# Kernel optimization log

Hardware: AMD Instinct MI355X
Metric: run time of the kernel (lower is better)

The kernel has to match this reference:

```python
import jax, jax.numpy as jnp
import numpy as np

D_MODEL = 1024
N_HEADS = 16
D_KV = 64
B, S = 2, 2048


def setup_inputs() -> dict:
    key = jax.random.key(0)
    ks = jax.random.split(key, 7)
    scale = 1.0 / np.sqrt(D_MODEL)
    return {
        "query": jax.random.normal(ks[0], (B, S, D_MODEL), jnp.float32),
        "key": jax.random.normal(ks[1], (B, S, D_MODEL), jnp.float32),
        "value": jax.random.normal(ks[2], (B, S, D_MODEL), jnp.float32),
        "mask": jnp.zeros((B, 1, 1, S), jnp.float32),
        "Wq": jax.random.normal(ks[3], (D_MODEL, N_HEADS * D_KV), jnp.float32) * scale,
        "Wk": jax.random.normal(ks[4], (D_MODEL, N_HEADS * D_KV), jnp.float32) * scale,
        "Wv": jax.random.normal(ks[5], (D_MODEL, N_HEADS * D_KV), jnp.float32) * scale,
        "Wo": jax.random.normal(ks[6], (N_HEADS * D_KV, D_MODEL), jnp.float32) * scale,
    }


def _split_heads(x):
    b, s, _ = x.shape
    return x.reshape(b, s, N_HEADS, D_KV).transpose(0, 2, 1, 3)  # [B,H,S,Dk]


def reference(query, key, value, mask, Wq, Wk, Wv, Wo):
    q = _split_heads(query @ Wq)
    k = _split_heads(key @ Wk)
    v = _split_heads(value @ Wv)
    scores = jnp.einsum("bhqd,bhkd->bhqk", q, k) / jnp.sqrt(
        jnp.asarray(D_KV, scores_dtype := q.dtype)
    )
    scores = scores + mask
    attn = jax.nn.softmax(scores, axis=-1)  # dropout_rate=0 -> identity
    ctx = jnp.einsum("bhqk,bhkd->bhqd", attn, v)
    ctx = ctx.transpose(0, 2, 1, 3).reshape(query.shape[0], -1, N_HEADS * D_KV)
    hidden = ctx @ Wo
    return hidden
```

## Files before the change

kernel.cpp:

```cpp
#include <hip/hip_runtime.h>
#include <hip/hip_bf16.h>
#include <stdint.h>

typedef __bf16 bf16;
typedef __bf16 bf16x8 __attribute__((ext_vector_type(8)));
typedef __bf16 bf16x4 __attribute__((ext_vector_type(4)));
typedef float  f32x4  __attribute__((ext_vector_type(4)));
typedef float  f32x16 __attribute__((ext_vector_type(16)));

#define S_LEN  2048
#define NH     16
#define DKV    64
#define DMODEL 1024
#define LOG2E  1.4426950408889634f

__device__ __forceinline__ void async_load16(const void* g, void* l) {
  __builtin_amdgcn_global_load_lds(
      (const __attribute__((address_space(1))) uint32_t*)(uintptr_t)g,
      (__attribute__((address_space(3))) uint32_t*)(uintptr_t)l,
      16, 0, 0);
}

__global__ void cast_qkv(const float* __restrict__ q, const float* __restrict__ k,
                         const float* __restrict__ v,
                         bf16* __restrict__ qo, bf16* __restrict__ ko, bf16* __restrict__ vo)
{
  int z = blockIdx.y;
  const float* in = (z == 0) ? q : (z == 1) ? k : v;
  bf16* out = (z == 0) ? qo : (z == 1) ? ko : vo;
  int i = blockIdx.x * 256 + threadIdx.x;
  const float4* in4 = (const float4*)in;
  float4 a = in4[2 * i];
  float4 c = in4[2 * i + 1];
  bf16x8 o;
  o[0] = (bf16)a.x; o[1] = (bf16)a.y; o[2] = (bf16)a.z; o[3] = (bf16)a.w;
  o[4] = (bf16)c.x; o[5] = (bf16)c.y; o[6] = (bf16)c.z; o[7] = (bf16)c.w;
  ((bf16x8*)out)[i] = o;
}

__global__ void transpose_w(const float* __restrict__ W0, const float* __restrict__ W1,
                            const float* __restrict__ W2, const float* __restrict__ W3,
                            bf16* __restrict__ T0, bf16* __restrict__ T1,
                            bf16* __restrict__ T2, bf16* __restrict__ T3)
{
  int z = blockIdx.z;
  const float* W = (z == 0) ? W0 : (z == 1) ? W1 : (z == 2) ? W2 : W3;
  bf16* T = (z == 0) ? T0 : (z == 1) ? T1 : (z == 2) ? T2 : T3;
  __shared__ float tile[32][33];
  int n0 = blockIdx.x * 32, k0 = blockIdx.y * 32;
  int tx = threadIdx.x, ty = threadIdx.y;
  for (int i = 0; i < 32; i += 8)
    tile[ty + i][tx] = W[(size_t)(k0 + ty + i) * DMODEL + n0 + tx];
  __syncthreads();
  for (int i = 0; i < 32; i += 8)
    T[(size_t)(n0 + ty + i) * DMODEL + k0 + tx] = (bf16)tile[tx][ty + i];
}

template<int TM, int MODE>
__global__ __launch_bounds__(256) void gemm_bt(
    const bf16* __restrict__ A0, const bf16* __restrict__ A1, const bf16* __restrict__ A2,
    const bf16* __restrict__ B0, const bf16* __restrict__ B1, const bf16* __restrict__ B2,
    void* __restrict__ C0, void* __restrict__ C1, void* __restrict__ C2,
    int M, int N, int K)
{
  constexpr int MI = TM / 32;
  __shared__ __align__(16) bf16 As[TM * 32];
  __shared__ __align__(16) bf16 Bs[128 * 32];
  int z = blockIdx.z;
  const bf16* A  = (z == 0) ? A0 : (z == 1) ? A1 : A2;
  const bf16* Bt = (z == 0) ? B0 : (z == 1) ? B1 : B2;
  void* C        = (z == 0) ? C0 : (z == 1) ? C1 : C2;

  const int m0 = blockIdx.y * TM;
  const int n0 = blockIdx.x * 128;
  const int tid = threadIdx.x;
  const int lane = tid & 63;
  const int wave = tid >> 6;
  const int wm = (wave >> 1) * (TM / 2);
  const int wn = (wave & 1) * 64;
  const int row = lane & 15;
  const int quad = lane >> 4;

  f32x4 acc[MI][4];
  for (int i = 0; i < MI; ++i)
    for (int j = 0; j < 4; ++j) acc[i][j] = (f32x4){0.f, 0.f, 0.f, 0.f};

  const int nk = K >> 5;
  for (int kt = 0; kt < nk; ++kt) {
    __syncthreads();
    const int kk = kt << 5;
    for (int j = 0; j < TM / 64; ++j) {
      int base = j * 256 + wave * 64;
      int idx = base + lane;
      int r = idx >> 2;
      int cb = (idx & 3) << 4;
      async_load16((const char*)(A + (size_t)(m0 + r) * K + kk) + cb,
                   (char*)As + (size_t)base * 16);
    }
    for (int j = 0; j < 2; ++j) {
      int base = j * 256 + wave * 64;
      int idx = base + lane;
      int r = idx >> 2;
      int cb = (idx & 3) << 4;
      async_load16((const char*)(Bt + (size_t)(n0 + r) * K + kk) + cb,
                   (char*)Bs + (size_t)base * 16);
    }
    __syncthreads();
    bf16x8 af[MI], bfr[4];
    for (int i = 0; i < MI; ++i)
      af[i] = *(const bf16x8*)(As + (wm + i * 16 + row) * 32 + quad * 8);
    for (int j = 0; j < 4; ++j)
      bfr[j] = *(const bf16x8*)(Bs + (wn + j * 16 + row) * 32 + quad * 8);
    for (int i = 0; i < MI; ++i)
      for (int j = 0; j < 4; ++j)
        acc[i][j] = __builtin_amdgcn_mfma_f32_16x16x32_bf16(af[i], bfr[j], acc[i][j], 0, 0, 0);
  }

  if (MODE == 0) {
    float* Cf = (float*)C;
    for (int i = 0; i < MI; ++i)
      for (int j = 0; j < 4; ++j)
        for (int r = 0; r < 4; ++r) {
          int gm = m0 + wm + i * 16 + quad * 4 + r;
          int gn = n0 + wn + j * 16 + row;
          Cf[(size_t)gm * N + gn] = acc[i][j][r];
        }
  } else if (z != 2) {
    bf16* Cb = (bf16*)C;
    for (int i = 0; i < MI; ++i)
      for (int j = 0; j < 4; ++j)
        for (int r = 0; r < 4; ++r) {
          int gm = m0 + wm + i * 16 + quad * 4 + r;
          int gn = n0 + wn + j * 16 + row;
          int b = gm >> 11, s = gm & 2047;
          int h = gn >> 6,  d = gn & 63;
          Cb[(((size_t)(b * NH + h)) * S_LEN + s) * DKV + d] = (bf16)acc[i][j][r];
        }
  } else {
    bf16* Cb = (bf16*)C;
    for (int i = 0; i < MI; ++i)
      for (int j = 0; j < 4; ++j) {
        int gm = m0 + wm + i * 16 + quad * 4;
        int gn = n0 + wn + j * 16 + row;
        int b = gm >> 11, s = gm & 2047;
        int h = gn >> 6,  d = gn & 63;
        int bh = b * NH + h;
        int tile = s >> 6, kb = (s & 63) >> 2;
        bf16x4 t;
        for (int r = 0; r < 4; ++r) t[r] = (bf16)acc[i][j][r];
        *(bf16x4*)(Cb + ((((size_t)bh * 32 + tile) * 16 + kb) * 64 + d) * 4) = t;
      }
  }
}

__global__ __launch_bounds__(256, 4) void attn_kernel(
    const bf16* __restrict__ Qh, const bf16* __restrict__ Kh, const bf16* __restrict__ Vperm,
    const float* __restrict__ mask, float* __restrict__ Opart, float* __restrict__ Lpart)
{
  __shared__ __align__(16) bf16 Ks[64 * 64];
  __shared__ __align__(16) bf16 Vts[64 * 64];
  __shared__ __align__(16) float masks2[64];

  const int bh = blockIdx.y;
  const int b = bh >> 4;
  const int q0 = blockIdx.x * 128;
  const int zh = blockIdx.z;
  const int tid = threadIdx.x;
  const int lane = tid & 63;
  const int wave = tid >> 6;
  const int ln = lane & 31;
  const int hi = lane >> 5;
  const float SC2 = 0.125f * LOG2E;

  const int qg = q0 + wave * 32 + ln;
  bf16x8 qf[4];
  {
    const bf16* qrow = Qh + ((size_t)bh * S_LEN + qg) * DKV;
    for (int c = 0; c < 4; ++c)
      qf[c] = *(const bf16x8*)(qrow + c * 16 + hi * 8);
  }

  f32x16 O[2];
  for (int nb = 0; nb < 2; ++nb)
    for (int i = 0; i < 16; ++i) O[nb][i] = 0.f;
  float lsum = 0.f;

  for (int it = 0; it < 16; ++it) {
    const int kv0 = zh * 1024 + it * 64;
    __syncthreads();
    const bf16* vtile = Vperm + ((size_t)bh * 32 + (kv0 >> 6)) * (64 * 64);
    for (int j = 0; j < 2; ++j) {
      int base = j * 256 + wave * 64;
      int idx = base + lane;
      int r = idx >> 3;
      int cc = (idx & 7) ^ (r & 7);
      async_load16(Kh + ((size_t)bh * S_LEN + kv0 + r) * DKV + cc * 8,
                   (char*)Ks + (size_t)base * 16);
      async_load16(vtile + (size_t)idx * 8,
                   (char*)Vts + (size_t)base * 16);
    }
    if (tid < 64) masks2[tid] = mask[b * S_LEN + kv0 + tid] * LOG2E;
    __syncthreads();

    f32x16 Sm[2];
    for (int i = 0; i < 16; ++i) { Sm[0][i] = 0.f; Sm[1][i] = 0.f; }
    for (int c = 0; c < 4; ++c) {
      bf16x8 k0 = *(const bf16x8*)(Ks + ln * 64        + (((2 * c + hi) ^ (ln & 7)) << 3));
      bf16x8 k1 = *(const bf16x8*)(Ks + (32 + ln) * 64 + (((2 * c + hi) ^ (ln & 7)) << 3));
      Sm[0] = __builtin_amdgcn_mfma_f32_32x32x16_bf16(k0, qf[c], Sm[0], 0, 0, 0);
      Sm[1] = __builtin_amdgcn_mfma_f32_32x32x16_bf16(k1, qf[c], Sm[1], 0, 0, 0);
    }

    for (int cg = 0; cg < 4; ++cg) {
      int mb = cg >> 1, g = cg & 1;
      int koff = 32 * mb + 16 * g + 4 * hi;
      f32x4 mklo = *(const f32x4*)(masks2 + koff);
      f32x4 mkhi = *(const f32x4*)(masks2 + koff + 8);
      bf16x8 ap;
      float ls0 = 0.f;
      for (int u = 0; u < 4; ++u) {
        float p = __builtin_amdgcn_exp2f(Sm[mb][g * 8 + u] * SC2 + mklo[u]);
        ls0 += p; ap[u] = (bf16)p;
      }
      for (int u = 0; u < 4; ++u) {
        float p = __builtin_amdgcn_exp2f(Sm[mb][g * 8 + 4 + u] * SC2 + mkhi[u]);
        ls0 += p; ap[4 + u] = (bf16)p;
      }
      lsum += ls0;
      int kb0 = hi + 4 * g + 8 * mb;
      for (int nb = 0; nb < 2; ++nb) {
        int d = nb * 32 + ln;
        bf16x4 lo = *(const bf16x4*)(Vts + ((size_t)kb0 * 64 + d) * 4);
        bf16x4 hv = *(const bf16x4*)(Vts + ((size_t)(kb0 + 2) * 64 + d) * 4);
        bf16x8 bv;
        for (int u = 0; u < 4; ++u) { bv[u] = lo[u]; bv[u + 4] = hv[u]; }
        O[nb] = __builtin_amdgcn_mfma_f32_32x32x16_bf16(ap, bv, O[nb], 0, 0, 0);
      }
    }
  }

  float lt = lsum + __shfl_xor(lsum, 32, 64);
  if (lane < 32)
    Lpart[((size_t)zh * 32 + bh) * S_LEN + q0 + wave * 32 + ln] = lt;

  float* ob = Opart + (((size_t)zh * 32 + bh) * S_LEN) * DKV;
  for (int g = 0; g < 4; ++g)
    for (int nb = 0; nb < 2; ++nb)
      for (int j = 0; j < 4; ++j) {
        int qrow = q0 + wave * 32 + j + 8 * g + 4 * hi;
        ob[(size_t)qrow * DKV + nb * 32 + ln] = O[nb][g * 4 + j];
      }
}

__global__ void combine_kernel(const float* __restrict__ Opart,
                               const float* __restrict__ Lpart,
                               bf16* __restrict__ ctx)
{
  int t = blockIdx.x * 256 + threadIdx.x;
  int dg = t & 15;
  int q  = (t >> 4) & 2047;
  int bh = t >> 15;
  int b = bh >> 4, h = bh & 15;
  size_t o0 = ((size_t)bh * S_LEN + q) * DKV + dg * 4;
  size_t o1 = ((size_t)(32 + bh) * S_LEN + q) * DKV + dg * 4;
  f32x4 a = *(const f32x4*)(Opart + o0);
  f32x4 c = *(const f32x4*)(Opart + o1);
  float l = Lpart[(size_t)bh * S_LEN + q] + Lpart[(size_t)(32 + bh) * S_LEN + q];
  float r = 1.0f / l;
  bf16x4 o;
  for (int u = 0; u < 4; ++u) o[u] = (bf16)((a[u] + c[u]) * r);
  *(bf16x4*)(ctx + ((size_t)(b * S_LEN + q)) * DMODEL + h * DKV + dg * 4) = o;
}

extern "C" void kernel_launch(void* const* d_in, const int* in_sizes, int n_in,
                              void* d_out, int out_size, void* d_ws, size_t ws_size,
                              hipStream_t stream)
{
  const float* query = (const float*)d_in[0];
  const float* key_  = (const float*)d_in[1];
  const float* value = (const float*)d_in[2];
  const float* mask  = (const float*)d_in[3];
  const float* Wq = (const float*)d_in[4];
  const float* Wk = (const float*)d_in[5];
  const float* Wv = (const float*)d_in[6];
  const float* Wo = (const float*)d_in[7];

  char* ws = (char*)d_ws;
  const size_t MB = (size_t)1 << 20;
  bf16* qb    = (bf16*)(ws + 0 * MB);
  bf16* kb    = (bf16*)(ws + 8 * MB);
  bf16* vb    = (bf16*)(ws + 16 * MB);
  bf16* wqt   = (bf16*)(ws + 24 * MB);
  bf16* wkt   = (bf16*)(ws + 26 * MB);
  bf16* wvt   = (bf16*)(ws + 28 * MB);
  bf16* qh    = (bf16*)(ws + 32 * MB);
  bf16* kh    = (bf16*)(ws + 40 * MB);
  bf16* vperm = (bf16*)(ws + 48 * MB);
  bf16* wot   = (bf16*)(ws + 56 * MB);
  float* Opart = (float*)(ws + 0 * MB);
  float* Lpart = (float*)(ws + 58 * MB);
  bf16* ctx   = (bf16*)(ws + 32 * MB);

  cast_qkv<<<dim3(2048, 3), 256, 0, stream>>>(query, key_, value, qb, kb, vb);
  transpose_w<<<dim3(32, 32, 4), dim3(32, 8), 0, stream>>>(Wq, Wk, Wv, Wo, wqt, wkt, wvt, wot);
  gemm_bt<128, 1><<<dim3(8, 32, 3), 256, 0, stream>>>(qb, kb, vb, wqt, wkt, wvt,
                                                      (void*)qh, (void*)kh, (void*)vperm,
                                                      4096, 1024, 1024);
  attn_kernel<<<dim3(16, 32, 2), 256, 0, stream>>>(qh, kh, vperm, mask, Opart, Lpart);
  combine_kernel<<<dim3(4096), 256, 0, stream>>>(Opart, Lpart, ctx);
  gemm_bt<64, 0><<<dim3(8, 64, 1), 256, 0, stream>>>(ctx, ctx, ctx, wot, wot, wot,
                                                     d_out, d_out, d_out,
                                                     4096, 1024, 1024);
}
```

Measured before the change: 231.4 us.

## Fuse split-KV combine into attention block and stage Q/K GEMM stores via LDS

The attention kernel now runs both KV halves inside one 512-thread block, one group of four waves per half. It combines the partial outputs and row sums through shared memory and writes normalized bf16 context directly. This removes the fp32 Opart/Lpart round trip through global memory and the separate combine kernel launch. Separately, the Q/K projection epilogue stages tiles in LDS so it can issue 16-byte coalesced stores into the head-split layout instead of scattered 2-byte writes. In exchange the attention grid has half as many blocks, each using more LDS and extra barriers, which may lower occupancy.

```diff
diff --git a/kernel.cpp b/kernel.cpp
--- a/kernel.cpp
+++ b/kernel.cpp
@@ -126,16 +126,28 @@
           Cf[(size_t)gm * N + gn] = acc[i][j][r];
         }
   } else if (z != 2) {
+    __shared__ __align__(16) bf16 Ls[64 * 132];
     bf16* Cb = (bf16*)C;
-    for (int i = 0; i < MI; ++i)
-      for (int j = 0; j < 4; ++j)
-        for (int r = 0; r < 4; ++r) {
-          int gm = m0 + wm + i * 16 + quad * 4 + r;
-          int gn = n0 + wn + j * 16 + row;
-          int b = gm >> 11, s = gm & 2047;
-          int h = gn >> 6,  d = gn & 63;
-          Cb[(((size_t)(b * NH + h)) * S_LEN + s) * DKV + d] = (bf16)acc[i][j][r];
-        }
+    const int bq = m0 >> 11;
+    for (int p = 0; p < 2; ++p) {
+      __syncthreads();
+      if ((wave >> 1) == p) {
+        for (int i = 0; i < MI; ++i)
+          for (int j = 0; j < 4; ++j)
+            for (int r = 0; r < 4; ++r)
+              Ls[(i * 16 + quad * 4 + r) * 132 + wn + j * 16 + row] = (bf16)acc[i][j][r];
+      }
+      __syncthreads();
+      for (int u = 0; u < 4; ++u) {
+        int cc = u * 256 + tid;
+        int rloc = cc >> 4, c8 = (cc & 15) * 8;
+        int s = (m0 + p * 64 + rloc) & 2047;
+        int gn = n0 + c8;
+        int h = gn >> 6, d = gn & 63;
+        bf16x8 val = *(const bf16x8*)(Ls + rloc * 132 + c8);
+        *(bf16x8*)(Cb + (((size_t)(bq * NH + h)) * S_LEN + s) * DKV + d) = val;
+      }
+    }
   } else {
     bf16* Cb = (bf16*)C;
     for (int i = 0; i < MI; ++i)
@@ -153,26 +165,32 @@
   }
 }
 
-__global__ __launch_bounds__(256, 4) void attn_kernel(
+__global__ __launch_bounds__(512, 4) void attn_kernel(
     const bf16* __restrict__ Qh, const bf16* __restrict__ Kh, const bf16* __restrict__ Vperm,
-    const float* __restrict__ mask, float* __restrict__ Opart, float* __restrict__ Lpart)
-{
-  __shared__ __align__(16) bf16 Ks[64 * 64];
-  __shared__ __align__(16) bf16 Vts[64 * 64];
-  __shared__ __align__(16) float masks2[64];
+    const float* __restrict__ mask, bf16* __restrict__ ctx)
+{
+  __shared__ __align__(16) bf16 KV[4 * 4096];
+  __shared__ __align__(16) float masks2[2 * 64];
+  __shared__ float Lhalf[8 * 32];
+  __shared__ float Lr[4 * 32];
 
   const int bh = blockIdx.y;
   const int b = bh >> 4;
+  const int h = bh & 15;
   const int q0 = blockIdx.x * 128;
-  const int zh = blockIdx.z;
   const int tid = threadIdx.x;
   const int lane = tid & 63;
   const int wave = tid >> 6;
+  const int w4 = wave & 3;
+  const int zh = wave >> 2;
   const int ln = lane & 31;
   const int hi = lane >> 5;
   const float SC2 = 0.125f * LOG2E;
 
-  const int qg = q0 + wave * 32 + ln;
+  bf16* Ksz  = KV + zh * 4096;
+  bf16* Vtsz = KV + 8192 + zh * 4096;
+
+  const int qg = q0 + w4 * 32 + ln;
   bf16x8 qf[4];
   {
     const bf16* qrow = Qh + ((size_t)bh * S_LEN + qg) * DKV;
@@ -188,32 +206,36 @@
   for (int it = 0; it < 16; ++it) {
     const int kv0 = zh * 1024 + it * 64;
     __syncthreads();
-    const bf16* vtile = Vperm + ((size_t)bh * 32 + (kv0 >> 6)) * (64 * 64);
+    const bf16* vtile = Vperm + ((size_t)bh * 32 + (kv0 >> 6)) * 4096;
     for (int j = 0; j < 2; ++j) {
-      int base = j * 256 + wave * 64;
+      int base = j * 256 + w4 * 64;
       int idx = base + lane;
       int r = idx >> 3;
       int cc = (idx & 7) ^ (r & 7);
       async_load16(Kh + ((size_t)bh * S_LEN + kv0 + r) * DKV + cc * 8,
-                   (char*)Ks + (size_t)base * 16);
+                   (char*)Ksz + (size_t)base * 16);
       async_load16(vtile + (size_t)idx * 8,
-                   (char*)Vts + (size_t)base * 16);
-    }
-    if (tid < 64) masks2[tid] = mask[b * S_LEN + kv0 + tid] * LOG2E;
+                   (char*)Vtsz + (size_t)base * 16);
+    }
+    if (tid < 128) {
+      int z2 = tid >> 6;
+      masks2[z2 * 64 + (tid & 63)] =
+          mask[b * S_LEN + z2 * 1024 + it * 64 + (tid & 63)] * LOG2E;
+    }
     __syncthreads();
 
     f32x16 Sm[2];
     for (int i = 0; i < 16; ++i) { Sm[0][i] = 0.f; Sm[1][i] = 0.f; }
     for (int c = 0; c < 4; ++c) {
-      bf16x8 k0 = *(const bf16x8*)(Ks + ln * 64        + (((2 * c + hi) ^ (ln & 7)) << 3));
-      bf16x8 k1 = *(const bf16x8*)(Ks + (32 + ln) * 64 + (((2 * c + hi) ^ (ln & 7)) << 3));
+      bf16x8 k0 = *(const bf16x8*)(Ksz + ln * 64        + (((2 * c + hi) ^ (ln & 7)) << 3));
+      bf16x8 k1 = *(const bf16x8*)(Ksz + (32 + ln) * 64 + (((2 * c + hi) ^ (ln & 7)) << 3));
       Sm[0] = __builtin_amdgcn_mfma_f32_32x32x16_bf16(k0, qf[c], Sm[0], 0, 0, 0);
       Sm[1] = __builtin_amdgcn_mfma_f32_32x32x16_bf16(k1, qf[c], Sm[1], 0, 0, 0);
     }
 
     for (int cg = 0; cg < 4; ++cg) {
       int mb = cg >> 1, g = cg & 1;
-      int koff = 32 * mb + 16 * g + 4 * hi;
+      int koff = zh * 64 + 32 * mb + 16 * g + 4 * hi;
       f32x4 mklo = *(const f32x4*)(masks2 + koff);
       f32x4 mkhi = *(const f32x4*)(masks2 + koff + 8);
       bf16x8 ap;
@@ -230,8 +252,8 @@
       int kb0 = hi + 4 * g + 8 * mb;
       for (int nb = 0; nb < 2; ++nb) {
         int d = nb * 32 + ln;
-        bf16x4 lo = *(const bf16x4*)(Vts + ((size_t)kb0 * 64 + d) * 4);
-        bf16x4 hv = *(const bf16x4*)(Vts + ((size_t)(kb0 + 2) * 64 + d) * 4);
+        bf16x4 lo = *(const bf16x4*)(Vtsz + ((size_t)kb0 * 64 + d) * 4);
+        bf16x4 hv = *(const bf16x4*)(Vtsz + ((size_t)(kb0 + 2) * 64 + d) * 4);
         bf16x8 bv;
         for (int u = 0; u < 4; ++u) { bv[u] = lo[u]; bv[u + 4] = hv[u]; }
         O[nb] = __builtin_amdgcn_mfma_f32_32x32x16_bf16(ap, bv, O[nb], 0, 0, 0);
@@ -240,36 +262,32 @@
   }
 
   float lt = lsum + __shfl_xor(lsum, 32, 64);
-  if (lane < 32)
-    Lpart[((size_t)zh * 32 + bh) * S_LEN + q0 + wave * 32 + ln] = lt;
-
-  float* ob = Opart + (((size_t)zh * 32 + bh) * S_LEN) * DKV;
-  for (int g = 0; g < 4; ++g)
-    for (int nb = 0; nb < 2; ++nb)
-      for (int j = 0; j < 4; ++j) {
-        int qrow = q0 + wave * 32 + j + 8 * g + 4 * hi;
-        ob[(size_t)qrow * DKV + nb * 32 + ln] = O[nb][g * 4 + j];
-      }
-}
-
-__global__ void combine_kernel(const float* __restrict__ Opart,
-                               const float* __restrict__ Lpart,
-                               bf16* __restrict__ ctx)
-{
-  int t = blockIdx.x * 256 + threadIdx.x;
-  int dg = t & 15;
-  int q  = (t >> 4) & 2047;
-  int bh = t >> 15;
-  int b = bh >> 4, h = bh & 15;
-  size_t o0 = ((size_t)bh * S_LEN + q) * DKV + dg * 4;
-  size_t o1 = ((size_t)(32 + bh) * S_LEN + q) * DKV + dg * 4;
-  f32x4 a = *(const f32x4*)(Opart + o0);
-  f32x4 c = *(const f32x4*)(Opart + o1);
-  float l = Lpart[(size_t)bh * S_LEN + q] + Lpart[(size_t)(32 + bh) * S_LEN + q];
-  float r = 1.0f / l;
-  bf16x4 o;
-  for (int u = 0; u < 4; ++u) o[u] = (bf16)((a[u] + c[u]) * r);
-  *(bf16x4*)(ctx + ((size_t)(b * S_LEN + q)) * DMODEL + h * DKV + dg * 4) = o;
+  __syncthreads();
+  if (lane < 32) Lhalf[wave * 32 + lane] = lt;
+  float* Op = (float*)KV;
+  if (zh == 1) {
+    float* ob = Op + w4 * 2048;
+    for (int g = 0; g < 4; ++g)
+      for (int nb = 0; nb < 2; ++nb)
+        for (int j = 0; j < 4; ++j)
+          ob[(j + 8 * g + 4 * hi) * 64 + nb * 32 + ln] = O[nb][g * 4 + j];
+  }
+  __syncthreads();
+  if (zh == 0) {
+    float lq = Lhalf[wave * 32 + ln] + Lhalf[(wave + 4) * 32 + ln];
+    Lr[wave * 32 + ln] = 1.0f / lq;
+    const float* ob = Op + wave * 2048;
+    __builtin_amdgcn_s_waitcnt(0);
+    for (int g = 0; g < 4; ++g) {
+      f32x4 ri = *(const f32x4*)(Lr + wave * 32 + g * 8 + hi * 4);
+      for (int nb = 0; nb < 2; ++nb)
+        for (int j = 0; j < 4; ++j) {
+          int qrow = q0 + wave * 32 + j + 8 * g + 4 * hi;
+          float v = (O[nb][g * 4 + j] + ob[(j + 8 * g + 4 * hi) * 64 + nb * 32 + ln]) * ri[j];
+          ctx[((size_t)b * S_LEN + qrow) * DMODEL + h * DKV + nb * 32 + ln] = (bf16)v;
+        }
+    }
+  }
 }
 
 extern "C" void kernel_launch(void* const* d_in, const int* in_sizes, int n_in,
@@ -293,21 +311,18 @@
   bf16* wqt   = (bf16*)(ws + 24 * MB);
   bf16* wkt   = (bf16*)(ws + 26 * MB);
   bf16* wvt   = (bf16*)(ws + 28 * MB);
+  bf16* wot   = (bf16*)(ws + 30 * MB);
   bf16* qh    = (bf16*)(ws + 32 * MB);
   bf16* kh    = (bf16*)(ws + 40 * MB);
   bf16* vperm = (bf16*)(ws + 48 * MB);
-  bf16* wot   = (bf16*)(ws + 56 * MB);
-  float* Opart = (float*)(ws + 0 * MB);
-  float* Lpart = (float*)(ws + 58 * MB);
-  bf16* ctx   = (bf16*)(ws + 32 * MB);
+  bf16* ctx   = (bf16*)(ws + 0 * MB);
 
   cast_qkv<<<dim3(2048, 3), 256, 0, stream>>>(query, key_, value, qb, kb, vb);
   transpose_w<<<dim3(32, 32, 4), dim3(32, 8), 0, stream>>>(Wq, Wk, Wv, Wo, wqt, wkt, wvt, wot);
   gemm_bt<128, 1><<<dim3(8, 32, 3), 256, 0, stream>>>(qb, kb, vb, wqt, wkt, wvt,
                                                       (void*)qh, (void*)kh, (void*)vperm,
                                                       4096, 1024, 1024);
-  attn_kernel<<<dim3(16, 32, 2), 256, 0, stream>>>(qh, kh, vperm, mask, Opart, Lpart);
-  combine_kernel<<<dim3(4096), 256, 0, stream>>>(Opart, Lpart, ctx);
+  attn_kernel<<<dim3(16, 32), 512, 0, stream>>>(qh, kh, vperm, mask, ctx);
   gemm_bt<64, 0><<<dim3(8, 64, 1), 256, 0, stream>>>(ctx, ctx, ctx, wot, wot, wot,
                                                      d_out, d_out, d_out,
                                                      4096, 1024, 1024);
```

Measured after the change: 232.6 us. About the same (+0.5%).

## Fuse input casts into QKV GEMM and split-KV combine into output GEMM

Applied to the files above, without the earlier changes.

Removes the separate fp32-to-bf16 cast kernel: the QKV projection GEMM now reads fp32 activations directly, converts them in registers and stores them to LDS. The split-KV combine kernel is folded into the output projection GEMM, which sums the two partial outputs and normalises them while loading its A tile. The Q/K head-layout epilogue is staged through LDS so global stores become 16-byte vectors. This cuts two launches and the intermediate bf16 traffic, at the cost of synchronous fp32 global loads in the GEMM main loops, which read twice as many bytes as before and are no longer async copies into LDS. The output GEMM also re-reads both fp32 partials for every N tile.

```diff
diff --git a/kernel.cpp b/kernel.cpp
--- a/kernel.cpp
+++ b/kernel.cpp
@@ -19,23 +19,6 @@
       (const __attribute__((address_space(1))) uint32_t*)(uintptr_t)g,
       (__attribute__((address_space(3))) uint32_t*)(uintptr_t)l,
       16, 0, 0);
-}
-
-__global__ void cast_qkv(const float* __restrict__ q, const float* __restrict__ k,
-                         const float* __restrict__ v,
-                         bf16* __restrict__ qo, bf16* __restrict__ ko, bf16* __restrict__ vo)
-{
-  int z = blockIdx.y;
-  const float* in = (z == 0) ? q : (z == 1) ? k : v;
-  bf16* out = (z == 0) ? qo : (z == 1) ? ko : vo;
-  int i = blockIdx.x * 256 + threadIdx.x;
-  const float4* in4 = (const float4*)in;
-  float4 a = in4[2 * i];
-  float4 c = in4[2 * i + 1];
-  bf16x8 o;
-  o[0] = (bf16)a.x; o[1] = (bf16)a.y; o[2] = (bf16)a.z; o[3] = (bf16)a.w;
-  o[4] = (bf16)c.x; o[5] = (bf16)c.y; o[6] = (bf16)c.z; o[7] = (bf16)c.w;
-  ((bf16x8*)out)[i] = o;
 }
 
 __global__ void transpose_w(const float* __restrict__ W0, const float* __restrict__ W1,
@@ -56,89 +39,94 @@
     T[(size_t)(n0 + ty + i) * DMODEL + k0 + tx] = (bf16)tile[tx][ty + i];
 }
 
-template<int TM, int MODE>
-__global__ __launch_bounds__(256) void gemm_bt(
-    const bf16* __restrict__ A0, const bf16* __restrict__ A1, const bf16* __restrict__ A2,
-    const bf16* __restrict__ B0, const bf16* __restrict__ B1, const bf16* __restrict__ B2,
-    void* __restrict__ C0, void* __restrict__ C1, void* __restrict__ C2,
-    int M, int N, int K)
-{
-  constexpr int MI = TM / 32;
-  __shared__ __align__(16) bf16 As[TM * 32];
-  __shared__ __align__(16) bf16 Bs[128 * 32];
-  int z = blockIdx.z;
-  const bf16* A  = (z == 0) ? A0 : (z == 1) ? A1 : A2;
-  const bf16* Bt = (z == 0) ? B0 : (z == 1) ? B1 : B2;
-  void* C        = (z == 0) ? C0 : (z == 1) ? C1 : C2;
-
-  const int m0 = blockIdx.y * TM;
+__global__ __launch_bounds__(256) void gemm_qkv(
+    const float* __restrict__ Aq, const float* __restrict__ Ak, const float* __restrict__ Av,
+    const bf16* __restrict__ Bq, const bf16* __restrict__ Bk, const bf16* __restrict__ Bv,
+    bf16* __restrict__ Cq, bf16* __restrict__ Ck, bf16* __restrict__ Cv)
+{
+  __shared__ __align__(16) char smem[64 * 132 * 2];
+  bf16* As = (bf16*)smem;
+  bf16* Bs = (bf16*)smem + 128 * 32;
+  bf16* Ls = (bf16*)smem;
+
+  const int z = blockIdx.z;
+  const float* A = (z == 0) ? Aq : (z == 1) ? Ak : Av;
+  const bf16* Bt = (z == 0) ? Bq : (z == 1) ? Bk : Bv;
+  bf16* C        = (z == 0) ? Cq : (z == 1) ? Ck : Cv;
+
+  const int m0 = blockIdx.y * 128;
   const int n0 = blockIdx.x * 128;
   const int tid = threadIdx.x;
   const int lane = tid & 63;
   const int wave = tid >> 6;
-  const int wm = (wave >> 1) * (TM / 2);
+  const int wm = (wave >> 1) * 64;
   const int wn = (wave & 1) * 64;
   const int row = lane & 15;
   const int quad = lane >> 4;
 
-  f32x4 acc[MI][4];
-  for (int i = 0; i < MI; ++i)
+  f32x4 acc[4][4];
+  for (int i = 0; i < 4; ++i)
     for (int j = 0; j < 4; ++j) acc[i][j] = (f32x4){0.f, 0.f, 0.f, 0.f};
 
-  const int nk = K >> 5;
-  for (int kt = 0; kt < nk; ++kt) {
-    __syncthreads();
+  const int ar = tid >> 2;
+  const int ac8 = (tid & 3) * 8;
+
+  for (int kt = 0; kt < 32; ++kt) {
     const int kk = kt << 5;
-    for (int j = 0; j < TM / 64; ++j) {
-      int base = j * 256 + wave * 64;
-      int idx = base + lane;
-      int r = idx >> 2;
-      int cb = (idx & 3) << 4;
-      async_load16((const char*)(A + (size_t)(m0 + r) * K + kk) + cb,
-                   (char*)As + (size_t)base * 16);
-    }
+    const float* s0p = A + (size_t)(m0 + ar) * DMODEL + kk + ac8;
+    const float* s1p = s0p + (size_t)64 * DMODEL;
+    f32x4 a00 = *(const f32x4*)s0p;
+    f32x4 a01 = *(const f32x4*)(s0p + 4);
+    f32x4 a10 = *(const f32x4*)s1p;
+    f32x4 a11 = *(const f32x4*)(s1p + 4);
+    __syncthreads();
     for (int j = 0; j < 2; ++j) {
       int base = j * 256 + wave * 64;
       int idx = base + lane;
       int r = idx >> 2;
       int cb = (idx & 3) << 4;
-      async_load16((const char*)(Bt + (size_t)(n0 + r) * K + kk) + cb,
+      async_load16((const char*)(Bt + (size_t)(n0 + r) * DMODEL + kk) + cb,
                    (char*)Bs + (size_t)base * 16);
     }
-    __syncthreads();
-    bf16x8 af[MI], bfr[4];
-    for (int i = 0; i < MI; ++i)
+    bf16x8 o0, o1;
+    for (int u = 0; u < 4; ++u) { o0[u] = (bf16)a00[u]; o0[u + 4] = (bf16)a01[u]; }
+    for (int u = 0; u < 4; ++u) { o1[u] = (bf16)a10[u]; o1[u + 4] = (bf16)a11[u]; }
+    *(bf16x8*)(As + ar * 32 + ac8) = o0;
+    *(bf16x8*)(As + (ar + 64) * 32 + ac8) = o1;
+    __syncthreads();
+    bf16x8 af[4], bfr[4];
+    for (int i = 0; i < 4; ++i)
       af[i] = *(const bf16x8*)(As + (wm + i * 16 + row) * 32 + quad * 8);
     for (int j = 0; j < 4; ++j)
       bfr[j] = *(const bf16x8*)(Bs + (wn + j * 16 + row) * 32 + quad * 8);
-    for (int i = 0; i < MI; ++i)
+    for (int i = 0; i < 4; ++i)
       for (int j = 0; j < 4; ++j)
         acc[i][j] = __builtin_amdgcn_mfma_f32_16x16x32_bf16(af[i], bfr[j], acc[i][j], 0, 0, 0);
   }
 
-  if (MODE == 0) {
-    float* Cf = (float*)C;
-    for (int i = 0; i < MI; ++i)
-      for (int j = 0; j < 4; ++j)
-        for (int r = 0; r < 4; ++r) {
-          int gm = m0 + wm + i * 16 + quad * 4 + r;
-          int gn = n0 + wn + j * 16 + row;
-          Cf[(size_t)gm * N + gn] = acc[i][j][r];
-        }
-  } else if (z != 2) {
-    bf16* Cb = (bf16*)C;
-    for (int i = 0; i < MI; ++i)
-      for (int j = 0; j < 4; ++j)
-        for (int r = 0; r < 4; ++r) {
-          int gm = m0 + wm + i * 16 + quad * 4 + r;
-          int gn = n0 + wn + j * 16 + row;
-          int b = gm >> 11, s = gm & 2047;
-          int h = gn >> 6,  d = gn & 63;
-          Cb[(((size_t)(b * NH + h)) * S_LEN + s) * DKV + d] = (bf16)acc[i][j][r];
-        }
+  if (z != 2) {
+    const int bq = m0 >> 11;
+    for (int p = 0; p < 2; ++p) {
+      __syncthreads();
+      if ((wave >> 1) == p) {
+        for (int i = 0; i < 4; ++i)
+          for (int j = 0; j < 4; ++j)
+            for (int r = 0; r < 4; ++r)
+              Ls[(i * 16 + quad * 4 + r) * 132 + wn + j * 16 + row] = (bf16)acc[i][j][r];
+      }
+      __syncthreads();
+      for (int u = 0; u < 4; ++u) {
+        int cc = u * 256 + tid;
+        int rloc = cc >> 4, c8 = (cc & 15) * 8;
+        int s = (m0 + p * 64 + rloc) & 2047;
+        int gn = n0 + c8;
+        int h = gn >> 6, d = gn & 63;
+        bf16x8 val = *(const bf16x8*)(Ls + rloc * 132 + c8);
+        *(bf16x8*)(C + (((size_t)(bq * NH + h)) * S_LEN + s) * DKV + d) = val;
+      }
+    }
   } else {
-    bf16* Cb = (bf16*)C;
-    for (int i = 0; i < MI; ++i)
+    for (int i = 0; i < 4; ++i)
       for (int j = 0; j < 4; ++j) {
         int gm = m0 + wm + i * 16 + quad * 4;
         int gn = n0 + wn + j * 16 + row;
@@ -148,7 +136,7 @@
         int tile = s >> 6, kb = (s & 63) >> 2;
         bf16x4 t;
         for (int r = 0; r < 4; ++r) t[r] = (bf16)acc[i][j][r];
-        *(bf16x4*)(Cb + ((((size_t)bh * 32 + tile) * 16 + kb) * 64 + d) * 4) = t;
+        *(bf16x4*)(C + ((((size_t)bh * 32 + tile) * 16 + kb) * 64 + d) * 4) = t;
       }
   }
 }
@@ -188,7 +176,7 @@
   for (int it = 0; it < 16; ++it) {
     const int kv0 = zh * 1024 + it * 64;
     __syncthreads();
-    const bf16* vtile = Vperm + ((size_t)bh * 32 + (kv0 >> 6)) * (64 * 64);
+    const bf16* vtile = Vperm + ((size_t)bh * 32 + (kv0 >> 6)) * 4096;
     for (int j = 0; j < 2; ++j) {
       int base = j * 256 + wave * 64;
       int idx = base + lane;
@@ -252,24 +240,83 @@
       }
 }
 
-__global__ void combine_kernel(const float* __restrict__ Opart,
-                               const float* __restrict__ Lpart,
-                               bf16* __restrict__ ctx)
-{
-  int t = blockIdx.x * 256 + threadIdx.x;
-  int dg = t & 15;
-  int q  = (t >> 4) & 2047;
-  int bh = t >> 15;
-  int b = bh >> 4, h = bh & 15;
-  size_t o0 = ((size_t)bh * S_LEN + q) * DKV + dg * 4;
-  size_t o1 = ((size_t)(32 + bh) * S_LEN + q) * DKV + dg * 4;
-  f32x4 a = *(const f32x4*)(Opart + o0);
-  f32x4 c = *(const f32x4*)(Opart + o1);
-  float l = Lpart[(size_t)bh * S_LEN + q] + Lpart[(size_t)(32 + bh) * S_LEN + q];
-  float r = 1.0f / l;
-  bf16x4 o;
-  for (int u = 0; u < 4; ++u) o[u] = (bf16)((a[u] + c[u]) * r);
-  *(bf16x4*)(ctx + ((size_t)(b * S_LEN + q)) * DMODEL + h * DKV + dg * 4) = o;
+__global__ __launch_bounds__(256) void gemm_out(
+    const float* __restrict__ Opart, const float* __restrict__ Lpart,
+    const bf16* __restrict__ Wot, float* __restrict__ Cout)
+{
+  __shared__ __align__(16) bf16 As[64 * 32];
+  __shared__ __align__(16) bf16 Bs[128 * 32];
+  __shared__ float rinv[NH * 64];
+
+  const int m0 = blockIdx.y * 64;
+  const int n0 = blockIdx.x * 128;
+  const int tid = threadIdx.x;
+  const int lane = tid & 63;
+  const int wave = tid >> 6;
+  const int wm = (wave >> 1) * 32;
+  const int wn = (wave & 1) * 64;
+  const int row = lane & 15;
+  const int quad = lane >> 4;
+  const int b = m0 >> 11;
+  const int s0 = m0 & 2047;
+
+  for (int u = 0; u < 4; ++u) {
+    int idx = u * 256 + tid;
+    int h = idx >> 6, r = idx & 63;
+    float l = Lpart[((size_t)(b * NH + h)) * S_LEN + s0 + r]
+            + Lpart[((size_t)(32 + b * NH + h)) * S_LEN + s0 + r];
+    rinv[idx] = 1.0f / l;
+  }
+
+  f32x4 acc[2][4];
+  for (int i = 0; i < 2; ++i)
+    for (int j = 0; j < 4; ++j) acc[i][j] = (f32x4){0.f, 0.f, 0.f, 0.f};
+
+  const int ar = tid >> 2;
+  const int ac8 = (tid & 3) * 8;
+
+  for (int kt = 0; kt < 32; ++kt) {
+    const int kk = kt << 5;
+    const int h = kk >> 6;
+    const int d0 = (kk & 63) + ac8;
+    const float* p0 = Opart + (((size_t)(b * NH + h)) * S_LEN + s0 + ar) * DKV + d0;
+    const float* p1 = Opart + (((size_t)(32 + b * NH + h)) * S_LEN + s0 + ar) * DKV + d0;
+    f32x4 a00 = *(const f32x4*)p0;
+    f32x4 a01 = *(const f32x4*)(p0 + 4);
+    f32x4 a10 = *(const f32x4*)p1;
+    f32x4 a11 = *(const f32x4*)(p1 + 4);
+    __syncthreads();
+    for (int j = 0; j < 2; ++j) {
+      int base = j * 256 + wave * 64;
+      int idx = base + lane;
+      int r = idx >> 2;
+      int cb = (idx & 3) << 4;
+      async_load16((const char*)(Wot + (size_t)(n0 + r) * DMODEL + kk) + cb,
+                   (char*)Bs + (size_t)base * 16);
+    }
+    float rv = rinv[h * 64 + ar];
+    bf16x8 o;
+    for (int u = 0; u < 4; ++u) o[u]     = (bf16)((a00[u] + a10[u]) * rv);
+    for (int u = 0; u < 4; ++u) o[u + 4] = (bf16)((a01[u] + a11[u]) * rv);
+    *(bf16x8*)(As + ar * 32 + ac8) = o;
+    __syncthreads();
+    bf16x8 af[2], bfr[4];
+    for (int i = 0; i < 2; ++i)
+      af[i] = *(const bf16x8*)(As + (wm + i * 16 + row) * 32 + quad * 8);
+    for (int j = 0; j < 4; ++j)
+      bfr[j] = *(const bf16x8*)(Bs + (wn + j * 16 + row) * 32 + quad * 8);
+    for (int i = 0; i < 2; ++i)
+      for (int j = 0; j < 4; ++j)
+        acc[i][j] = __builtin_amdgcn_mfma_f32_16x16x32_bf16(af[i], bfr[j], acc[i][j], 0, 0, 0);
+  }
+
+  for (int i = 0; i < 2; ++i)
+    for (int j = 0; j < 4; ++j)
+      for (int r = 0; r < 4; ++r) {
+        int gm = m0 + wm + i * 16 + quad * 4 + r;
+        int gn = n0 + wn + j * 16 + row;
+        Cout[(size_t)gm * DMODEL + gn] = acc[i][j][r];
+      }
 }
 
 extern "C" void kernel_launch(void* const* d_in, const int* in_sizes, int n_in,
@@ -287,28 +334,19 @@
 
   char* ws = (char*)d_ws;
   const size_t MB = (size_t)1 << 20;
-  bf16* qb    = (bf16*)(ws + 0 * MB);
-  bf16* kb    = (bf16*)(ws + 8 * MB);
-  bf16* vb    = (bf16*)(ws + 16 * MB);
-  bf16* wqt   = (bf16*)(ws + 24 * MB);
-  bf16* wkt   = (bf16*)(ws + 26 * MB);
-  bf16* wvt   = (bf16*)(ws + 28 * MB);
-  bf16* qh    = (bf16*)(ws + 32 * MB);
-  bf16* kh    = (bf16*)(ws + 40 * MB);
-  bf16* vperm = (bf16*)(ws + 48 * MB);
-  bf16* wot   = (bf16*)(ws + 56 * MB);
-  float* Opart = (float*)(ws + 0 * MB);
+  bf16* qh    = (bf16*)(ws + 0 * MB);
+  bf16* kh    = (bf16*)(ws + 8 * MB);
+  bf16* vperm = (bf16*)(ws + 16 * MB);
+  bf16* wot   = (bf16*)(ws + 24 * MB);
+  float* Opart = (float*)(ws + 26 * MB);
+  bf16* wqt   = (bf16*)(ws + 26 * MB);
+  bf16* wkt   = (bf16*)(ws + 28 * MB);
+  bf16* wvt   = (bf16*)(ws + 30 * MB);
   float* Lpart = (float*)(ws + 58 * MB);
-  bf16* ctx   = (bf16*)(ws + 32 * MB);
-
-  cast_qkv<<<dim3(2048, 3), 256, 0, stream>>>(query, key_, value, qb, kb, vb);
+
   transpose_w<<<dim3(32, 32, 4), dim3(32, 8), 0, stream>>>(Wq, Wk, Wv, Wo, wqt, wkt, wvt, wot);
-  gemm_bt<128, 1><<<dim3(8, 32, 3), 256, 0, stream>>>(qb, kb, vb, wqt, wkt, wvt,
-                                                      (void*)qh, (void*)kh, (void*)vperm,
-                                                      4096, 1024, 1024);
+  gemm_qkv<<<dim3(8, 32, 3), 256, 0, stream>>>(query, key_, value, wqt, wkt, wvt,
+                                               qh, kh, vperm);
   attn_kernel<<<dim3(16, 32, 2), 256, 0, stream>>>(qh, kh, vperm, mask, Opart, Lpart);
-  combine_kernel<<<dim3(4096), 256, 0, stream>>>(Opart, Lpart, ctx);
-  gemm_bt<64, 0><<<dim3(8, 64, 1), 256, 0, stream>>>(ctx, ctx, ctx, wot, wot, wot,
-                                                     d_out, d_out, d_out,
-                                                     4096, 1024, 1024);
-}
+  gemm_out<<<dim3(8, 64), 256, 0, stream>>>(Opart, Lpart, wot, (float*)d_out);
+}
```

Result: slower. 249.7 us (+7.9%).
